# Kernel optimization log

Measured on AMD Instinct MI355X. Metric: run time of the kernel, lower is better.

Reference implementation:

```python
import jax, jax.numpy as jnp
import numpy as np

ROPE_BASE = 10000
B, L, D, NH = 2, 2048, 1024, 16
HD = D // NH


def apply_rope(inputs, positions, base_frequency):
    # inputs: [B, L, N, H], positions: [L]
    head_dim = inputs.shape[-1]
    fraction = 2 * jnp.arange(0, head_dim // 2) / head_dim
    timescale = base_frequency ** fraction  # [H/2]
    sinusoid = positions[..., None] / timescale[None, None, :]  # [1, L, H/2]
    sinusoid = sinusoid[..., None, :]  # [1, L, 1, H/2]
    sin, cos = jnp.sin(sinusoid), jnp.cos(sinusoid)
    first, second = jnp.split(inputs, 2, axis=-1)
    out = jnp.concatenate([first * cos - second * sin,
                           second * cos + first * sin], axis=-1)
    return out.astype(inputs.dtype)


def setup_inputs() -> dict:
    key = jax.random.key(0)
    ks = jax.random.split(key, 5)
    s = 0.02
    return {
        "x": jax.random.normal(ks[0], (B, L, D), jnp.float32),
        "wq_w": jax.random.normal(ks[1], (D, D), jnp.float32) * s,
        "wq_b": jnp.zeros((D,), jnp.float32),
        "wk_w": jax.random.normal(ks[2], (D, D), jnp.float32) * s,
        "wk_b": jnp.zeros((D,), jnp.float32),
        "wv_w": jax.random.normal(ks[3], (D, D), jnp.float32) * s,
        "wv_b": jnp.zeros((D,), jnp.float32),
        "wo_w": jax.random.normal(ks[4], (D, D), jnp.float32) * s,
        "wo_b": jnp.zeros((D,), jnp.float32),
    }


def reference(x, wq_w, wq_b, wk_w, wk_b, wv_w, wv_b, wo_w, wo_b):
    b, l, _ = x.shape
    q = (x @ wq_w + wq_b).reshape(b, l, NH, HD)
    k = (x @ wk_w + wk_b).reshape(b, l, NH, HD)
    v = (x @ wv_w + wv_b).reshape(b, l, NH, HD)
    pos = jnp.arange(l)
    q = apply_rope(q, pos, ROPE_BASE)
    k = apply_rope(k, pos, ROPE_BASE)
    # [B, N, L, H]
    q = q.transpose(0, 2, 1, 3)
    k = k.transpose(0, 2, 1, 3)
    v = v.transpose(0, 2, 1, 3)
    scale = jnp.sqrt(jnp.asarray(HD, q.dtype))
    scores = jnp.einsum('bnqh,bnkh->bnqk', q, k) / scale  # [B, N, L, L]
    causal = jnp.tril(jnp.ones((l, l), bool))
    scores = jnp.where(causal, scores, jnp.finfo(scores.dtype).min)
    attn = jax.nn.softmax(scores, axis=-1)
    ctx = jnp.einsum('bnqk,bnkh->bnqh', attn, v)
    ctx = ctx.transpose(0, 2, 1, 3).reshape(b, l, D)
    return ctx @ wo_w + wo_b
```

## Files before the change

kernel.cpp:

```cpp
#include <hip/hip_runtime.h>
#include <hip/hip_bf16.h>
#include <float.h>
#include <math.h>

#define BB  2
#define LLEN 2048
#define DD  1024
#define NHH 16
#define HDD 64
#define MROWS (BB * LLEN)

typedef __bf16 bf16x8  __attribute__((ext_vector_type(8)));
typedef float  f32x4   __attribute__((ext_vector_type(4)));
typedef float  f32x16  __attribute__((ext_vector_type(16)));
typedef ushort us8     __attribute__((ext_vector_type(8)));

#define EXP2F(x) __builtin_amdgcn_exp2f(x)

static __device__ __forceinline__ ushort f2bf(float f) {
    __hip_bfloat16 h = __float2bfloat16(f);
    return *reinterpret_cast<ushort*>(&h);
}
static __device__ __forceinline__ float bfu(ushort u) {
    unsigned x = (unsigned)u << 16;
    return __uint_as_float(x);
}
static __device__ __forceinline__ unsigned pack2(float a, float b) {
    return (unsigned)f2bf(a) | ((unsigned)f2bf(b) << 16);
}

__device__ __forceinline__ void gload16(const void* g, void* l) {
    __builtin_amdgcn_global_load_lds(
        (const __attribute__((address_space(1))) void*)g,
        (__attribute__((address_space(3))) void*)l, 16, 0, 0);
}

__global__ __launch_bounds__(256) void cvt_x_k(const float* __restrict__ in,
                                               ushort* __restrict__ out) {
    int idx = blockIdx.x * 256 + threadIdx.x;
    float4 v = reinterpret_cast<const float4*>(in)[idx];
    ushort4 o;
    o.x = f2bf(v.x); o.y = f2bf(v.y); o.z = f2bf(v.z); o.w = f2bf(v.w);
    reinterpret_cast<ushort4*>(out)[idx] = o;
}

__global__ __launch_bounds__(256) void wt_cvt_all_k(const float* __restrict__ w0,
                                                    const float* __restrict__ w1,
                                                    const float* __restrict__ w2,
                                                    const float* __restrict__ w3,
                                                    ushort* __restrict__ qkv,
                                                    ushort* __restrict__ wo) {
    __shared__ float T[64][65];
    const int z = blockIdx.z;
    const float* in = (z == 0) ? w0 : (z == 1) ? w1 : (z == 2) ? w2 : w3;
    ushort* out = (z < 3) ? (qkv + (size_t)z * 1024 * DD) : wo;

    const int r0 = blockIdx.y * 64, c0 = blockIdx.x * 64;
    const int tid = threadIdx.x;
    for (int i = tid; i < 64 * 16; i += 256) {
        int r = i >> 4, c4 = (i & 15) * 4;
        float4 v = *reinterpret_cast<const float4*>(&in[(size_t)(r0 + r) * DD + c0 + c4]);
        T[r][c4 + 0] = v.x; T[r][c4 + 1] = v.y; T[r][c4 + 2] = v.z; T[r][c4 + 3] = v.w;
    }
    __syncthreads();
    for (int i = tid; i < 64 * 16; i += 256) {
        int rr = i >> 4, cc4 = (i & 15) * 4;
        ushort4 o;
        o.x = f2bf(T[cc4 + 0][rr]);
        o.y = f2bf(T[cc4 + 1][rr]);
        o.z = f2bf(T[cc4 + 2][rr]);
        o.w = f2bf(T[cc4 + 3][rr]);
        *reinterpret_cast<ushort4*>(&out[(size_t)(c0 + rr) * DD + r0 + cc4]) = o;
    }
}

template <int MODE>
__global__ __launch_bounds__(256, 3) void gemm_mfma_k(
    const __bf16* __restrict__ A, const __bf16* __restrict__ Bt,
    const float* __restrict__ bias0, const float* __restrict__ bias1,
    const float* __restrict__ bias2,
    float* __restrict__ out_f32,
    __hip_bfloat16* __restrict__ oq, __hip_bfloat16* __restrict__ ok,
    __hip_bfloat16* __restrict__ ov) {
    constexpr int K  = DD;
    constexpr int NF = (MODE == 1) ? 8 : 4;
    constexpr int BN = NF * 16;
    constexpr int HALF = (64 + BN) * 64;
    __shared__ char smem[2 * HALF * 2];
    __bf16* smem_e = (__bf16*)smem;

    const int tid  = threadIdx.x;
    const int w    = tid >> 6;
    const int lane = tid & 63;
    const int lr   = lane & 15;
    const int lg   = lane >> 4;
    const int bm = blockIdx.y * 64, bn = blockIdx.x * BN;

    const int srow8 = lane >> 3;
    const int schk  = (lane & 7) ^ srow8;
    const __bf16* gA = A  + (size_t)(bm + w * 16 + srow8) * K + schk * 8;
    const __bf16* gB = Bt + (size_t)(bn + w * (NF * 4) + srow8) * K + schk * 8;

    f32x4 acc[NF] = {};
    const int l7 = lr & 7;

    auto STAGE = [&](int buf, int k0) {
        __bf16* base = smem_e + buf * HALF;
        char* lA = (char*)base + w * 16 * 128;
        char* lB = (char*)(base + 4096) + w * (NF * 4) * 128;
#pragma unroll
        for (int c = 0; c < 2; ++c)
            gload16(gA + (size_t)(c * 8) * K + k0, lA + c * 1024);
#pragma unroll
        for (int c = 0; c < NF / 2; ++c)
            gload16(gB + (size_t)(c * 8) * K + k0, lB + c * 1024);
    };

    STAGE(0, 0);
    __syncthreads();
    for (int i = 0; i < 16; ++i) {
        if (i < 15) STAGE((i + 1) & 1, (i + 1) * 64);
        const __bf16* As_ = smem_e + (i & 1) * HALF;
        const __bf16* Bs_ = As_ + 4096;
#pragma unroll
        for (int kk = 0; kk < 2; ++kk) {
            const int rchk = ((kk * 4 + lg) ^ l7) << 3;
            bf16x8 a = *reinterpret_cast<const bf16x8*>(As_ + (w * 16 + lr) * 64 + rchk);
#pragma unroll
            for (int n = 0; n < NF; ++n) {
                bf16x8 b = *reinterpret_cast<const bf16x8*>(Bs_ + (n * 16 + lr) * 64 + rchk);
                acc[n] = __builtin_amdgcn_mfma_f32_16x16x32_bf16(a, b, acc[n], 0, 0, 0);
            }
        }
        __syncthreads();
    }

    if (MODE == 1) {
        const int seg = bn >> 10;
        const int colbase = bn & 1023;
        const int h0 = colbase >> 6;
        const int b  = bm >> 11;
        const int bmL = bm & 2047;
        if (seg == 2) {
#pragma unroll
            for (int n = 0; n < NF; ++n) {
                const int h  = h0 + (n >> 2);
                const int hd = (n & 3) * 16 + lr;
                const float bv = bias2[colbase + n * 16 + lr];
                const int rowb = bm + w * 16 + lg * 4;
                const int l0 = rowb & 2047;
                ushort4 st;
                st.x = f2bf(acc[n][0] + bv);
                st.y = f2bf(acc[n][1] + bv);
                st.z = f2bf(acc[n][2] + bv);
                st.w = f2bf(acc[n][3] + bv);
                const int bh = b * NHH + h;
                const int t  = l0 >> 5;
                const int j  = ((hd >> 5) << 1) | ((l0 >> 4) & 1);
                const int ln = (hd & 31) + ((l0 >> 3) & 1) * 32;
                const int e0 = l0 & 7;
                size_t base = ((((size_t)bh * 64 + t) * 4 + j) * 64 + ln) * 8 + e0;
                *reinterpret_cast<ushort4*>(&ov[base]) = st;
            }
        } else {
            const float* biasp = (seg == 0) ? bias0 : bias1;
            const float osc = (seg == 0) ? 0.18033688011112042f : 1.0f;
            ushort* LP = (ushort*)smem + w * 2048;
#pragma unroll
            for (int hh = 0; hh < 2; ++hh) {
#pragma unroll
                for (int n2 = 0; n2 < 2; ++n2) {
                    const int nA = hh * 4 + n2, nB = nA + 2;
                    const int d  = n2 * 16 + lr;
                    const float tsd = exp2f((float)d * -0.4152410118609203f);
                    const float bv0 = biasp[colbase + hh * 64 + d];
                    const float bv1 = biasp[colbase + hh * 64 + d + 32];
                    const int c0  = d >> 4;
                    const int hi8 = (d >> 3) & 1;
#pragma unroll
                    for (int i = 0; i < 4; ++i) {
                        const int lw = lg * 4 + i;
                        const int l  = bmL + w * 16 + lw;
                        float s, c;
                        __sincosf((float)l * tsd, &s, &c);
                        const float x0 = acc[nA][i] + bv0;
                        const float x1 = acc[nB][i] + bv1;
                        const int lnL = lw + 16 * hi8;
                        LP[hh * 1024 + (c0 * 32 + lnL) * 8 + (d & 7)] =
                            f2bf((x0 * c - x1 * s) * osc);
                        LP[hh * 1024 + ((c0 + 2) * 32 + lnL) * 8 + (d & 7)] =
                            f2bf((x1 * c + x0 * s) * osc);
                    }
                }
            }
            __syncthreads();
            ushort* dstp = (ushort*)((seg == 0) ? oq : ok);
            const int t   = (bmL >> 5) + (w >> 1);
            const int r0w = (w & 1) * 16;
#pragma unroll
            for (int hh = 0; hh < 2; ++hh) {
                const int bh = b * NHH + h0 + hh;
#pragma unroll
                for (int it = 0; it < 2; ++it) {
                    const int f = it * 64 + lane;
                    const int c = f >> 5, lnL = f & 31;
                    const int ln = r0w + (lnL & 15) + 32 * (lnL >> 4);
                    us8 v = *reinterpret_cast<const us8*>(&LP[hh * 1024 + f * 8]);
                    size_t base = ((((size_t)bh * 64 + t) * 4 + c) * 64 + ln) * 8;
                    *reinterpret_cast<us8*>(&dstp[base]) = v;
                }
            }
        }
    } else {
        float* FP = (float*)smem + w * 1024;
        __syncthreads();
#pragma unroll
        for (int n = 0; n < NF; ++n) {
            const int col = n * 16 + lr;
            const float bv = bias0[bn + col];
#pragma unroll
            for (int i = 0; i < 4; ++i)
                FP[(lg * 4 + i) * 64 + col] = acc[n][i] + bv;
        }
        __syncthreads();
#pragma unroll
        for (int it = 0; it < 4; ++it) {
            const int f = it * 64 + lane;
            const int row16 = f >> 4, cq = f & 15;
            float4 v = *reinterpret_cast<const float4*>(&FP[row16 * 64 + cq * 4]);
            const int row = bm + w * 16 + row16;
            *reinterpret_cast<float4*>(&out_f32[(size_t)row * DD + bn + cq * 4]) = v;
        }
    }
}

#define ATTN_LOAD(KF, VF, T0)                                                   \
    do {                                                                        \
        const __bf16* kp_ = kbase + (size_t)(T0) * 2048;                        \
        KF[0] = *reinterpret_cast<const bf16x8*>(kp_);                          \
        KF[1] = *reinterpret_cast<const bf16x8*>(kp_ + 512);                    \
        KF[2] = *reinterpret_cast<const bf16x8*>(kp_ + 1024);                   \
        KF[3] = *reinterpret_cast<const bf16x8*>(kp_ + 1536);                   \
        const __bf16* vp_ = vbase + (size_t)(T0) * 2048;                        \
        VF[0] = *reinterpret_cast<const bf16x8*>(vp_);                          \
        VF[1] = *reinterpret_cast<const bf16x8*>(vp_ + 512);                    \
        VF[2] = *reinterpret_cast<const bf16x8*>(vp_ + 1024);                   \
        VF[3] = *reinterpret_cast<const bf16x8*>(vp_ + 1536);                   \
    } while (0)

#define ATTN_TILE(KF, VF, T0, MASKIT, QG)                                       \
    do {                                                                        \
        f32x16 s_ = {};                                                         \
        __builtin_amdgcn_s_setprio(1);                                          \
        s_ = __builtin_amdgcn_mfma_f32_32x32x16_bf16(KF[0], qf[0], s_, 0, 0, 0);\
        s_ = __builtin_amdgcn_mfma_f32_32x32x16_bf16(KF[1], qf[1], s_, 0, 0, 0);\
        s_ = __builtin_amdgcn_mfma_f32_32x32x16_bf16(KF[2], qf[2], s_, 0, 0, 0);\
        s_ = __builtin_amdgcn_mfma_f32_32x32x16_bf16(KF[3], qf[3], s_, 0, 0, 0);\
        __builtin_amdgcn_s_setprio(0);                                          \
        float p_[16];                                                           \
        const int k0_ = (T0) * 32;                                              \
        if (MASKIT) {                                                           \
            _Pragma("unroll")                                                   \
            for (int i = 0; i < 16; ++i) {                                      \
                int kkg_ = k0_ + (i & 3) + 8 * (i >> 2) + 4 * hi;               \
                p_[i] = (kkg_ <= (QG)) ? EXP2F(s_[i]) : 0.f;                    \
            }                                                                   \
        } else {                                                                \
            _Pragma("unroll")                                                   \
            for (int i = 0; i < 16; ++i) p_[i] = EXP2F(s_[i]);                  \
        }                                                                       \
        _Pragma("unroll")                                                       \
        for (int i = 0; i < 16; ++i) lsum += p_[i];                             \
        unsigned u_[8], x_[8];                                                  \
        _Pragma("unroll")                                                       \
        for (int j = 0; j < 8; ++j)                                             \
            u_[j] = pack2(p_[2 * j], p_[2 * j + 1]);                            \
        _Pragma("unroll")                                                       \
        for (int j = 0; j < 8; ++j)                                             \
            x_[j] = (unsigned)__shfl_xor((int)u_[j], 32);                       \
        union { unsigned d[4]; bf16x8 v; } B1_, B2_;                            \
        if (hi == 0) {                                                          \
            B1_.d[0] = u_[0]; B1_.d[1] = u_[1]; B1_.d[2] = x_[0]; B1_.d[3] = x_[1]; \
            B2_.d[0] = u_[4]; B2_.d[1] = u_[5]; B2_.d[2] = x_[4]; B2_.d[3] = x_[5]; \
        } else {                                                                \
            B1_.d[0] = x_[2]; B1_.d[1] = x_[3]; B1_.d[2] = u_[2]; B1_.d[3] = u_[3]; \
            B2_.d[0] = x_[6]; B2_.d[1] = x_[7]; B2_.d[2] = u_[6]; B2_.d[3] = u_[7]; \
        }                                                                       \
        __builtin_amdgcn_s_setprio(1);                                          \
        o0 = __builtin_amdgcn_mfma_f32_32x32x16_bf16(VF[0], B1_.v, o0, 0, 0, 0);\
        o0 = __builtin_amdgcn_mfma_f32_32x32x16_bf16(VF[1], B2_.v, o0, 0, 0, 0);\
        o1 = __builtin_amdgcn_mfma_f32_32x32x16_bf16(VF[2], B1_.v, o1, 0, 0, 0);\
        o1 = __builtin_amdgcn_mfma_f32_32x32x16_bf16(VF[3], B2_.v, o1, 0, 0, 0);\
        __builtin_amdgcn_s_setprio(0);                                          \
    } while (0)

__global__ __launch_bounds__(256) void attn_mfma17_k(const __bf16* __restrict__ Qp,
                                                     const __bf16* __restrict__ Kp,
                                                     const __bf16* __restrict__ Vp,
                                                     __hip_bfloat16* __restrict__ ctx) {
    __shared__ ushort oLs[4][64][34];
    __shared__ float lvL[4][64];

    const int tid  = threadIdx.x;
    const int w    = tid >> 6;
    const int lane = tid & 63;
    const int q32  = lane & 31;
    const int hi   = lane >> 5;

    const int bid = blockIdx.x;
    const int g_  = (bid & 7) * 256 + (bid >> 3);
    const int bh  = g_ >> 6;
    const int qt  = 63 - (g_ & 63);
    const int qg  = qt * 32 + q32;

    const __bf16* qbase = Qp + (size_t)bh * (64 * 4 * 512) + lane * 8;
    const __bf16* kbase = Kp + (size_t)bh * (64 * 4 * 512) + lane * 8;
    const __bf16* vbase = Vp + (size_t)bh * (64 * 4 * 512) + lane * 8;

    const int b = bh >> 4, h = bh & 15;

    bf16x8 qf[4];
    const __bf16* qp_ = qbase + (size_t)qt * 2048;
    qf[0] = *reinterpret_cast<const bf16x8*>(qp_);
    qf[1] = *reinterpret_cast<const bf16x8*>(qp_ + 512);
    qf[2] = *reinterpret_cast<const bf16x8*>(qp_ + 1024);
    qf[3] = *reinterpret_cast<const bf16x8*>(qp_ + 1536);

    f32x16 o0 = {}, o1 = {};
    float lsum = 0.f;

    bf16x8 kf[4], vf[4];
    for (int t = w; t <= qt; t += 4) {
        ATTN_LOAD(kf, vf, t);
        ATTN_TILE(kf, vf, t, t == qt, qg);
    }

#pragma unroll
    for (int r = 0; r < 16; r += 2) {
        *reinterpret_cast<unsigned*>(&oLs[w][lane][r])      = pack2(o0[r], o0[r + 1]);
        *reinterpret_cast<unsigned*>(&oLs[w][lane][16 + r]) = pack2(o1[r], o1[r + 1]);
    }
    lvL[w][lane] = lsum;
    __syncthreads();

    float Lt = 0.f;
#pragma unroll
    for (int j = 0; j < 4; ++j)
        Lt += lvL[j][q32] + lvL[j][q32 + 32];
    const float inv = 1.0f / Lt;

    __hip_bfloat16* dst = ctx + ((size_t)(b * LLEN + qg)) * DD + h * HDD;
    const int T = w >> 1;
    const int gb = (w & 1) * 2;
#pragma unroll
    for (int g2 = 0; g2 < 2; ++g2) {
        const int g = gb + g2;
        const int rb = T * 16 + 4 * g;
        float acc4[4] = {0.f, 0.f, 0.f, 0.f};
#pragma unroll
        for (int j = 0; j < 4; ++j) {
            unsigned a = *reinterpret_cast<const unsigned*>(&oLs[j][lane][rb]);
            unsigned c = *reinterpret_cast<const unsigned*>(&oLs[j][lane][rb + 2]);
            acc4[0] += bfu((ushort)(a & 0xffff));
            acc4[1] += bfu((ushort)(a >> 16));
            acc4[2] += bfu((ushort)(c & 0xffff));
            acc4[3] += bfu((ushort)(c >> 16));
        }
        ushort st4[4];
#pragma unroll
        for (int e = 0; e < 4; ++e) st4[e] = f2bf(acc4[e] * inv);
        const int d = T * 32 + 8 * g + 4 * hi;
        *reinterpret_cast<ushort4*>(dst + d) = *reinterpret_cast<ushort4*>(st4);
    }
}

extern "C" void kernel_launch(void* const* d_in, const int* in_sizes, int n_in,
                              void* d_out, int out_size, void* d_ws, size_t ws_size,
                              hipStream_t stream) {
    const float* x    = (const float*)d_in[0];
    const float* wq_w = (const float*)d_in[1];
    const float* wq_b = (const float*)d_in[2];
    const float* wk_w = (const float*)d_in[3];
    const float* wk_b = (const float*)d_in[4];
    const float* wv_w = (const float*)d_in[5];
    const float* wv_b = (const float*)d_in[6];
    const float* wo_w = (const float*)d_in[7];
    const float* wo_b = (const float*)d_in[8];
    float* out = (float*)d_out;

    const size_t MB = 1024 * 1024;
    char* p = (char*)d_ws;
    __bf16* x16   = (__bf16*)p;            p += 8 * MB;
    __bf16* wqkvt = (__bf16*)p;            p += 6 * MB;
    __bf16* wot   = (__bf16*)p;            p += 2 * MB;
    __hip_bfloat16* qp16 = (__hip_bfloat16*)p; p += 8 * MB;
    __hip_bfloat16* kp16 = (__hip_bfloat16*)p; p += 8 * MB;
    __hip_bfloat16* vp16 = (__hip_bfloat16*)p; p += 8 * MB;
    __hip_bfloat16* ctx16 = (__hip_bfloat16*)p;

    hipLaunchKernelGGL(cvt_x_k, dim3(4096), dim3(256), 0, stream, x, (ushort*)x16);
    hipLaunchKernelGGL(wt_cvt_all_k, dim3(16, 16, 4), dim3(256), 0, stream,
                       wq_w, wk_w, wv_w, wo_w, (ushort*)wqkvt, (ushort*)wot);

    hipLaunchKernelGGL((gemm_mfma_k<1>), dim3(24, 64), dim3(256), 0, stream,
                       x16, wqkvt, wq_b, wk_b, wv_b, (float*)nullptr, qp16, kp16, vp16);

    hipLaunchKernelGGL(attn_mfma17_k, dim3(2048), dim3(256), 0, stream,
                       (const __bf16*)qp16, (const __bf16*)kp16, (const __bf16*)vp16, ctx16);

    hipLaunchKernelGGL((gemm_mfma_k<0>), dim3(16, 64), dim3(256), 0, stream,
                       (const __bf16*)ctx16, wot, wo_b, (const float*)nullptr, (const float*)nullptr,
                       out, (__hip_bfloat16*)nullptr, (__hip_bfloat16*)nullptr, (__hip_bfloat16*)nullptr);
}
```

Measured before the change: 100.8 us.

## Triple-buffer GEMM K-loop with vmcnt waits and fuse x conversion into weight kernel

The GEMM main loop moves from double to triple buffering in LDS, prefetching two K-tiles ahead. It replaces __syncthreads with explicit s_waitcnt vmcnt counts plus s_barrier, so loads can stay in flight across iterations. Launch bounds drop from 3 to 2 blocks per CU to make room for the larger shared memory. Separately, the x fp32-to-bf16 conversion is folded into the weight transpose kernel as an extra z-slice, removing one kernel launch. The risks are lower occupancy and hand-counted vmcnt values that must match the number of outstanding loads.

```diff
diff --git a/kernel.cpp b/kernel.cpp
--- a/kernel.cpp
+++ b/kernel.cpp
@@ -35,28 +35,35 @@
         (__attribute__((address_space(3))) void*)l, 16, 0, 0);
 }
 
-__global__ __launch_bounds__(256) void cvt_x_k(const float* __restrict__ in,
-                                               ushort* __restrict__ out) {
-    int idx = blockIdx.x * 256 + threadIdx.x;
-    float4 v = reinterpret_cast<const float4*>(in)[idx];
-    ushort4 o;
-    o.x = f2bf(v.x); o.y = f2bf(v.y); o.z = f2bf(v.z); o.w = f2bf(v.w);
-    reinterpret_cast<ushort4*>(out)[idx] = o;
-}
-
 __global__ __launch_bounds__(256) void wt_cvt_all_k(const float* __restrict__ w0,
                                                     const float* __restrict__ w1,
                                                     const float* __restrict__ w2,
                                                     const float* __restrict__ w3,
+                                                    const float* __restrict__ xin,
                                                     ushort* __restrict__ qkv,
-                                                    ushort* __restrict__ wo) {
+                                                    ushort* __restrict__ wo,
+                                                    ushort* __restrict__ xout) {
+    const int z = blockIdx.z;
+    const int tid = threadIdx.x;
+    if (z == 4) {
+        const int bx = blockIdx.y * 16 + blockIdx.x;
+        const float4* src = reinterpret_cast<const float4*>(xin);
+        ushort4* dst = reinterpret_cast<ushort4*>(xout);
+        const int base = bx * 4096 + tid;
+#pragma unroll
+        for (int it = 0; it < 16; ++it) {
+            float4 v = src[base + it * 256];
+            ushort4 o;
+            o.x = f2bf(v.x); o.y = f2bf(v.y); o.z = f2bf(v.z); o.w = f2bf(v.w);
+            dst[base + it * 256] = o;
+        }
+        return;
+    }
     __shared__ float T[64][65];
-    const int z = blockIdx.z;
     const float* in = (z == 0) ? w0 : (z == 1) ? w1 : (z == 2) ? w2 : w3;
     ushort* out = (z < 3) ? (qkv + (size_t)z * 1024 * DD) : wo;
 
     const int r0 = blockIdx.y * 64, c0 = blockIdx.x * 64;
-    const int tid = threadIdx.x;
     for (int i = tid; i < 64 * 16; i += 256) {
         int r = i >> 4, c4 = (i & 15) * 4;
         float4 v = *reinterpret_cast<const float4*>(&in[(size_t)(r0 + r) * DD + c0 + c4]);
@@ -75,7 +82,7 @@
 }
 
 template <int MODE>
-__global__ __launch_bounds__(256, 3) void gemm_mfma_k(
+__global__ __launch_bounds__(256, 2) void gemm_mfma_k(
     const __bf16* __restrict__ A, const __bf16* __restrict__ Bt,
     const float* __restrict__ bias0, const float* __restrict__ bias1,
     const float* __restrict__ bias2,
@@ -86,7 +93,7 @@
     constexpr int NF = (MODE == 1) ? 8 : 4;
     constexpr int BN = NF * 16;
     constexpr int HALF = (64 + BN) * 64;
-    __shared__ char smem[2 * HALF * 2];
+    __shared__ char smem[3 * HALF * 2];
     __bf16* smem_e = (__bf16*)smem;
 
     const int tid  = threadIdx.x;
@@ -117,10 +124,17 @@
     };
 
     STAGE(0, 0);
-    __syncthreads();
+    STAGE(1, 64);
+    if constexpr (MODE == 1)
+        asm volatile("s_waitcnt vmcnt(6)" ::: "memory");
+    else
+        asm volatile("s_waitcnt vmcnt(4)" ::: "memory");
+    __builtin_amdgcn_s_barrier();
+
+#pragma unroll 1
     for (int i = 0; i < 16; ++i) {
-        if (i < 15) STAGE((i + 1) & 1, (i + 1) * 64);
-        const __bf16* As_ = smem_e + (i & 1) * HALF;
+        if (i + 2 < 16) STAGE((i + 2) % 3, (i + 2) * 64);
+        const __bf16* As_ = smem_e + (i % 3) * HALF;
         const __bf16* Bs_ = As_ + 4096;
 #pragma unroll
         for (int kk = 0; kk < 2; ++kk) {
@@ -132,7 +146,15 @@
                 acc[n] = __builtin_amdgcn_mfma_f32_16x16x32_bf16(a, b, acc[n], 0, 0, 0);
             }
         }
-        __syncthreads();
+        if (i + 2 < 16) {
+            if constexpr (MODE == 1)
+                asm volatile("s_waitcnt vmcnt(6)" ::: "memory");
+            else
+                asm volatile("s_waitcnt vmcnt(4)" ::: "memory");
+        } else if (i + 1 < 16) {
+            asm volatile("s_waitcnt vmcnt(0)" ::: "memory");
+        }
+        __builtin_amdgcn_s_barrier();
     }
 
     if (MODE == 1) {
@@ -398,9 +420,9 @@
     __hip_bfloat16* vp16 = (__hip_bfloat16*)p; p += 8 * MB;
     __hip_bfloat16* ctx16 = (__hip_bfloat16*)p;
 
-    hipLaunchKernelGGL(cvt_x_k, dim3(4096), dim3(256), 0, stream, x, (ushort*)x16);
-    hipLaunchKernelGGL(wt_cvt_all_k, dim3(16, 16, 4), dim3(256), 0, stream,
-                       wq_w, wk_w, wv_w, wo_w, (ushort*)wqkvt, (ushort*)wot);
+    hipLaunchKernelGGL(wt_cvt_all_k, dim3(16, 16, 5), dim3(256), 0, stream,
+                       wq_w, wk_w, wv_w, wo_w, x,
+                       (ushort*)wqkvt, (ushort*)wot, (ushort*)x16);
 
     hipLaunchKernelGGL((gemm_mfma_k<1>), dim3(24, 64), dim3(256), 0, stream,
                        x16, wqkvt, wq_b, wk_b, wv_b, (float*)nullptr, qp16, kp16, vp16);
```

Result: slower. 104.6 us (+3.8%).
